# Kernel optimization log

Measured on AMD Instinct MI355X. Metric: run time of the kernel, lower is better.

Reference implementation:

```python
import jax, jax.numpy as jnp
import numpy as np

DIM_PROBLEM = 8192
DIM_CONTEXT = 512
DIM_HIDDEN = 1024


def setup_inputs() -> dict:
    key = jax.random.key(0)
    ks = jax.random.split(key, 8)
    s = 0.02
    H, C = DIM_HIDDEN, DIM_CONTEXT
    return {
        "context": jax.random.normal(ks[0], (C,), jnp.float32),
        # linear_1: dim_context -> 1
        "W1": jax.random.normal(ks[1], (1, C), jnp.float32) * s,
        "b1": jnp.zeros((1,), jnp.float32),
        # LSTM layer 0 (input dim 1), torch gate order [i, f, g, o]
        "Wih0": jax.random.normal(ks[2], (4 * H, 1), jnp.float32) * s,
        "Whh0": jax.random.normal(ks[3], (4 * H, H), jnp.float32) * s,
        "bih0": jnp.zeros((4 * H,), jnp.float32),
        "bhh0": jnp.zeros((4 * H,), jnp.float32),
        # LSTM layer 1 (input dim H)
        "Wih1": jax.random.normal(ks[4], (4 * H, H), jnp.float32) * s,
        "Whh1": jax.random.normal(ks[5], (4 * H, H), jnp.float32) * s,
        "bih1": jnp.zeros((4 * H,), jnp.float32),
        "bhh1": jnp.zeros((4 * H,), jnp.float32),
        # linear_2: dim_hidden -> 1
        "W2": jax.random.normal(ks[6], (1, H), jnp.float32) * s,
        "b2": jnp.zeros((1,), jnp.float32),
    }


def _lstm_cell(gin, h, c, Whh, b):
    # gin = W_ih @ x (precomputed); torch gate order i, f, g, o
    gates = gin + Whh @ h + b
    i, f, g, o = jnp.split(gates, 4)
    i, f, o = jax.nn.sigmoid(i), jax.nn.sigmoid(f), jax.nn.sigmoid(o)
    g = jnp.tanh(g)
    c = f * c + i * g
    return o * jnp.tanh(c), c


def reference(context, W1, b1, Wih0, Whh0, bih0, bhh0, Wih1, Whh1, bih1, bhh1, W2, b2):
    H = Whh0.shape[1]
    x0 = (W1 @ context + b1)[0]  # linear_1 seeds the first LSTM input (scalar)
    b0 = bih0 + bhh0
    b1g = bih1 + bhh1
    keys = jax.random.split(jax.random.key(42), DIM_PROBLEM)

    def step(carry, k):
        h0, c0, h1, c1, x, logp = carry
        h0, c0 = _lstm_cell(Wih0[:, 0] * x, h0, c0, Whh0, b0)
        h1, c1 = _lstm_cell(Wih1 @ h0, h1, c1, Whh1, b1g)
        p = jax.nn.sigmoid(W2 @ h1 + b2)[0]
        # Bernoulli sample; detached as in the original (.clone().detach(), .item())
        s = jax.lax.stop_gradient(jax.random.bernoulli(k, p).astype(jnp.float32))
        # log of running product  p^s * (1-p)^(1-s)
        logp = logp + s * jnp.log(p) + (1.0 - s) * jnp.log1p(-p)
        return (h0, c0, h1, c1, s, logp), s

    z = jnp.zeros((H,), jnp.float32)
    carry0 = (z, z, z, z, x0, jnp.float32(0.0))
    (_, _, _, _, _, logp), solution = jax.lax.scan(step, carry0, keys)
    return solution, logp
```

## Files before the change

kernel.cpp:

```cpp
#include <hip/hip_runtime.h>
#include <stdint.h>
#include <math.h>


#define H     1024
#define NSTEP 8192
#define NWG   512
#define BLK   64
#define NROW  25

typedef _Float16 h2 __attribute__((ext_vector_type(2)));
typedef _Float16 h8 __attribute__((ext_vector_type(8)));

union U32H2 { uint32_t u; h2 v; };

__device__ __forceinline__ unsigned long long pack_vt(float v0, float v1, uint32_t tag){
  U32H2 p; p.v.x = (_Float16)v0; p.v.y = (_Float16)v1;
  return ((unsigned long long)tag << 32) | (unsigned long long)p.u;
}

__device__ __forceinline__ uint2 tf2x32(uint32_t k0, uint32_t k1, uint32_t x0, uint32_t x1){
  uint32_t k2 = k0 ^ k1 ^ 0x1BD11BDAu;
  x0 += k0; x1 += k1;
#define TFR(r) { x0 += x1; x1 = (x1 << (r)) | (x1 >> (32 - (r))); x1 ^= x0; }
  TFR(13) TFR(15) TFR(26) TFR(6)
  x0 += k1; x1 += k2 + 1u;
  TFR(17) TFR(29) TFR(16) TFR(24)
  x0 += k2; x1 += k0 + 2u;
  TFR(13) TFR(15) TFR(26) TFR(6)
  x0 += k0; x1 += k1 + 3u;
  TFR(17) TFR(29) TFR(16) TFR(24)
  x0 += k1; x1 += k2 + 4u;
  TFR(13) TFR(15) TFR(26) TFR(6)
  x0 += k2; x1 += k0 + 5u;
#undef TFR
  uint2 r; r.x = x0; r.y = x1; return r;
}

__device__ __forceinline__ uint32_t jax_word(uint32_t i){
  return (i < 8192u) ? tf2x32(0u, 42u, i, i + 8192u).x
                     : tf2x32(0u, 42u, i - 8192u, i).y;
}

__device__ __forceinline__ float wred64(float x){
  #pragma unroll
  for(int off = 32; off > 0; off >>= 1) x += __shfl_xor(x, off, 64);
  return x;
}

#if __has_builtin(__builtin_amdgcn_fdot2)
__device__ __forceinline__ float fdot2f(h2 a, h2 b, float c){ return __builtin_amdgcn_fdot2(a, b, c, false); }
#else
__device__ __forceinline__ float fdot2f(h2 a, h2 b, float c){
  return (float)a.x * (float)b.x + (float)a.y * (float)b.y + c;
}
#endif

__device__ __forceinline__ float sigm(float x){
  x = fminf(fmaxf(x, -30.f), 30.f);
  return 1.f / (1.f + __expf(-x));
}
__device__ __forceinline__ float tanh_f(float x){
  x = fminf(fmaxf(x, -15.f), 15.f);
  float e = __expf(2.f * x);
  return (e - 1.f) / (e + 1.f);
}

__device__ __forceinline__ unsigned long long ld_slot(const unsigned long long* p){
  return __hip_atomic_load((unsigned long long*)p, __ATOMIC_RELAXED, __HIP_MEMORY_SCOPE_AGENT);
}

__device__ __forceinline__ void poll_h(const unsigned long long* __restrict__ buf,
                                       uint32_t tag, int lane, h2* hv){
  const unsigned long long* p0 = buf + (lane << 2);
  const unsigned long long* p1 = buf + 256 + (lane << 2);
  unsigned long long pv[8];
  #pragma unroll
  for(int k = 0; k < 4; k++) pv[k]     = ld_slot(p0 + k);
  #pragma unroll
  for(int k = 0; k < 4; k++) pv[4 + k] = ld_slot(p1 + k);
  #pragma unroll
  for(int k = 0; k < 8; k++){
    const unsigned long long* p = (k < 4) ? (p0 + k) : (p1 + (k - 4));
    while((uint32_t)(pv[k] >> 32) != tag){
      __builtin_amdgcn_s_sleep(1);
      pv[k] = ld_slot(p);
    }
  }
  #pragma unroll
  for(int k = 0; k < 8; k++){
    U32H2 u; u.u = (uint32_t)pv[k];
    hv[k] = u.v;
  }
}

__device__ __forceinline__ float row_part(const h2* __restrict__ wrow, int lane, const h2* hv){
  h8 wl = *(const h8*)(wrow + (lane << 2));
  h8 wh = *(const h8*)(wrow + 256 + (lane << 2));
  float a0 = 0.f, a1 = 0.f;
  h2 w;
  w = __builtin_shufflevector(wl, wl, 0, 1); a0 = fdot2f(w, hv[0], a0);
  w = __builtin_shufflevector(wl, wl, 2, 3); a1 = fdot2f(w, hv[1], a1);
  w = __builtin_shufflevector(wl, wl, 4, 5); a0 = fdot2f(w, hv[2], a0);
  w = __builtin_shufflevector(wl, wl, 6, 7); a1 = fdot2f(w, hv[3], a1);
  w = __builtin_shufflevector(wh, wh, 0, 1); a0 = fdot2f(w, hv[4], a0);
  w = __builtin_shufflevector(wh, wh, 2, 3); a1 = fdot2f(w, hv[5], a1);
  w = __builtin_shufflevector(wh, wh, 4, 5); a0 = fdot2f(w, hv[6], a0);
  w = __builtin_shufflevector(wh, wh, 6, 7); a1 = fdot2f(w, hv[7], a1);
  return a0 + a1;
}

__global__ void __launch_bounds__(BLK)
lstm_persist(const float* __restrict__ ctx,  const float* __restrict__ W1p,  const float* __restrict__ b1p,
             const float* __restrict__ Wih0, const float* __restrict__ Whh0,
             const float* __restrict__ bih0, const float* __restrict__ bhh0,
             const float* __restrict__ Wih1, const float* __restrict__ Whh1,
             const float* __restrict__ bih1, const float* __restrict__ bhh1,
             const float* __restrict__ W2p,  const float* __restrict__ b2p,
             float* __restrict__ out,
             unsigned long long* __restrict__ h0buf,
             unsigned long long* __restrict__ h1buf)
{
  __shared__ h2 w[NROW][H/2];

  const int lane = threadIdx.x;
  const int wg   = blockIdx.x;
  const int j0   = wg << 1;

  #pragma unroll 1
  for(int r = 0; r < NROW; r++){
    const float* rowp;
    if(r < 8)      { int g = r & 3,        j = j0 + (r >> 2);        rowp = Wih1 + (size_t)(g*H + j)*H; }
    else if(r < 16){ int rr = r - 8;  int g = rr & 3, j = j0 + (rr >> 2); rowp = Whh0 + (size_t)(g*H + j)*H; }
    else if(r < 24){ int rr = r - 16; int g = rr & 3, j = j0 + (rr >> 2); rowp = Whh1 + (size_t)(g*H + j)*H; }
    else           rowp = W2p;
    const float4* s4 = (const float4*)rowp;
    #pragma unroll
    for(int it = 0; it < 4; it++){
      float4 f = s4[lane + (it << 6)];
      h2 pa; pa.x = (_Float16)f.x; pa.y = (_Float16)f.y;
      h2 pb; pb.x = (_Float16)f.z; pb.y = (_Float16)f.w;
      const int ci = (lane + (it << 6)) << 1;
      w[r][ci] = pa; w[r][ci + 1] = pb;
    }
  }
  __syncthreads();

  float b0g[8], b1g[8], w0g[8];
  #pragma unroll
  for(int e = 0; e < 2; e++){
    const int j = j0 + e;
    #pragma unroll
    for(int g = 0; g < 4; g++){
      b0g[4*e + g] = bih0[g*H + j] + bhh0[g*H + j];
      b1g[4*e + g] = bih1[g*H + j] + bhh1[g*H + j];
      w0g[4*e + g] = Wih0[g*H + j];
    }
  }
  const float b2v = b2p[0];

  float xacc = 0.f;
  for(int c = lane; c < 512; c += 64) xacc += W1p[c] * ctx[c];
  const float x0 = wred64(xacc) + b1p[0];

  float c0[2], c1[2] = {0.f, 0.f}, logp = 0.f;
  float a0[8];
  float a1[8] = {0.f,0.f,0.f,0.f,0.f,0.f,0.f,0.f};

  {
    float h0v[2];
    #pragma unroll
    for(int e = 0; e < 2; e++){
      float gi = sigm (w0g[4*e+0]*x0 + b0g[4*e+0]);
      float gf = sigm (w0g[4*e+1]*x0 + b0g[4*e+1]);
      float gg = tanh_f(w0g[4*e+2]*x0 + b0g[4*e+2]);
      float go = sigm (w0g[4*e+3]*x0 + b0g[4*e+3]);
      c0[e] = gi * gg;
      h0v[e] = go * tanh_f(c0[e]);
    }
    if(lane == 0)
      __hip_atomic_store(&h0buf[wg], pack_vt(h0v[0], h0v[1], 1u),
                         __ATOMIC_RELAXED, __HIP_MEMORY_SCOPE_AGENT);
  }

  h2 hv[8];
  float u = 0.f;

  #pragma unroll 1
  for(int t = 0; t < NSTEP; t++){
    const uint32_t tt = (uint32_t)t;

    poll_h(h0buf, tt + 1u, lane, hv);

    float s1[8];
    #pragma unroll
    for(int r = 0; r < 8; r++) s1[r] = row_part(&w[r][0], lane, hv);
    #pragma unroll
    for(int off = 32; off > 0; off >>= 1){
      #pragma unroll
      for(int r = 0; r < 8; r++) s1[r] += __shfl_xor(s1[r], off, 64);
    }
    {
      float h1v[2];
      #pragma unroll
      for(int e = 0; e < 2; e++){
        float gi = sigm (s1[4*e+0] + a1[4*e+0] + b1g[4*e+0]);
        float gf = sigm (s1[4*e+1] + a1[4*e+1] + b1g[4*e+1]);
        float gg = tanh_f(s1[4*e+2] + a1[4*e+2] + b1g[4*e+2]);
        float go = sigm (s1[4*e+3] + a1[4*e+3] + b1g[4*e+3]);
        c1[e] = gf*c1[e] + gi*gg;
        h1v[e] = go * tanh_f(c1[e]);
      }
      if(lane == 0)
        __hip_atomic_store(&h1buf[wg], pack_vt(h1v[0], h1v[1], tt + 1u),
                           __ATOMIC_RELAXED, __HIP_MEMORY_SCOPE_AGENT);
    }

    {
      const uint32_t kk0 = jax_word(2u*tt), kk1 = jax_word(2u*tt + 1u);
      const uint32_t bits = tf2x32(kk0, kk1, 0u, 0u).x;
      u = __uint_as_float((bits >> 9) | 0x3f800000u) - 1.0f;
    }
    float sa[8];
    #pragma unroll
    for(int r = 0; r < 8; r++) sa[r] = row_part(&w[8 + r][0], lane, hv);
    #pragma unroll
    for(int off = 32; off > 0; off >>= 1){
      #pragma unroll
      for(int r = 0; r < 8; r++) sa[r] += __shfl_xor(sa[r], off, 64);
    }
    #pragma unroll
    for(int r = 0; r < 8; r++) a0[r] = sa[r];

    poll_h(h1buf, tt + 1u, lane, hv);

    float z = row_part(&w[24][0], lane, hv);
    z = wred64(z) + b2v;
    const float p = sigm(z);
    const float s = (u < p) ? 1.f : 0.f;
    logp += s * __logf(p) + (1.f - s) * __logf(1.f - p);
    if(wg == 0 && lane == 0) out[t] = s;
    {
      float h0v[2];
      #pragma unroll
      for(int e = 0; e < 2; e++){
        float gi = sigm (a0[4*e+0] + w0g[4*e+0]*s + b0g[4*e+0]);
        float gf = sigm (a0[4*e+1] + w0g[4*e+1]*s + b0g[4*e+1]);
        float gg = tanh_f(a0[4*e+2] + w0g[4*e+2]*s + b0g[4*e+2]);
        float go = sigm (a0[4*e+3] + w0g[4*e+3]*s + b0g[4*e+3]);
        c0[e] = gf*c0[e] + gi*gg;
        h0v[e] = go * tanh_f(c0[e]);
      }
      if(lane == 0)
        __hip_atomic_store(&h0buf[wg], pack_vt(h0v[0], h0v[1], tt + 2u),
                           __ATOMIC_RELAXED, __HIP_MEMORY_SCOPE_AGENT);
    }

    float sb[8];
    #pragma unroll
    for(int r = 0; r < 8; r++) sb[r] = row_part(&w[16 + r][0], lane, hv);
    #pragma unroll
    for(int off = 32; off > 0; off >>= 1){
      #pragma unroll
      for(int r = 0; r < 8; r++) sb[r] += __shfl_xor(sb[r], off, 64);
    }
    #pragma unroll
    for(int r = 0; r < 8; r++) a1[r] = sb[r];
  }

  if(wg == 0 && lane == 0) out[NSTEP] = logp;
}

extern "C" void kernel_launch(void* const* d_in, const int* in_sizes, int n_in,
                              void* d_out, int out_size, void* d_ws, size_t ws_size,
                              hipStream_t stream){
  unsigned long long* h0buf = (unsigned long long*)d_ws;
  unsigned long long* h1buf = h0buf + 512;
  hipLaunchKernelGGL(lstm_persist, dim3(NWG), dim3(BLK), 0, stream,
    (const float*)d_in[0],  (const float*)d_in[1],  (const float*)d_in[2],
    (const float*)d_in[3],  (const float*)d_in[4],  (const float*)d_in[5],  (const float*)d_in[6],
    (const float*)d_in[7],  (const float*)d_in[8],  (const float*)d_in[9],  (const float*)d_in[10],
    (const float*)d_in[11], (const float*)d_in[12],
    (float*)d_out, h0buf, h1buf);
}
```

Baseline: 33.45 ms.

## Speculate layer-0 state for both sample outcomes to remove one grid sync per step

Each step, every workgroup now computes the next layer-0 hidden state for both possible Bernoulli outcomes (s=0 and s=1) and publishes both copies, tagged, to double-buffered slots. After the sample is drawn, each workgroup picks the matching copy. This takes the layer-0 exchange off the serial chain from h1 to the sample, so each step needs one cross-workgroup wait on the critical path instead of two. The Wih1·h0 and Whh1·h1 matvecs are also merged into a single reduction. In exchange, layer-0 gate math is done twice and more global slots are polled per step.

```diff
diff --git a/kernel.cpp b/kernel.cpp
--- a/kernel.cpp
+++ b/kernel.cpp
@@ -70,6 +70,28 @@
   return __hip_atomic_load((unsigned long long*)p, __ATOMIC_RELAXED, __HIP_MEMORY_SCOPE_AGENT);
 }
 
+__device__ __forceinline__ void spin8(unsigned long long* pv,
+                                      const unsigned long long* p0,
+                                      const unsigned long long* p1,
+                                      uint32_t tag){
+  #pragma unroll
+  for(int k = 0; k < 8; k++){
+    const unsigned long long* p = (k < 4) ? (p0 + k) : (p1 + (k - 4));
+    while((uint32_t)(pv[k] >> 32) != tag){
+      __builtin_amdgcn_s_sleep(1);
+      pv[k] = ld_slot(p);
+    }
+  }
+}
+
+__device__ __forceinline__ void unpack8(const unsigned long long* pv, h2* hv){
+  #pragma unroll
+  for(int k = 0; k < 8; k++){
+    U32H2 u; u.u = (uint32_t)pv[k];
+    hv[k] = u.v;
+  }
+}
+
 __device__ __forceinline__ void poll_h(const unsigned long long* __restrict__ buf,
                                        uint32_t tag, int lane, h2* hv){
   const unsigned long long* p0 = buf + (lane << 2);
@@ -79,19 +101,8 @@
   for(int k = 0; k < 4; k++) pv[k]     = ld_slot(p0 + k);
   #pragma unroll
   for(int k = 0; k < 4; k++) pv[4 + k] = ld_slot(p1 + k);
-  #pragma unroll
-  for(int k = 0; k < 8; k++){
-    const unsigned long long* p = (k < 4) ? (p0 + k) : (p1 + (k - 4));
-    while((uint32_t)(pv[k] >> 32) != tag){
-      __builtin_amdgcn_s_sleep(1);
-      pv[k] = ld_slot(p);
-    }
-  }
-  #pragma unroll
-  for(int k = 0; k < 8; k++){
-    U32H2 u; u.u = (uint32_t)pv[k];
-    hv[k] = u.v;
-  }
+  spin8(pv, p0, p1, tag);
+  unpack8(pv, hv);
 }
 
 __device__ __forceinline__ float row_part(const h2* __restrict__ wrow, int lane, const h2* hv){
@@ -118,8 +129,9 @@
              const float* __restrict__ bih1, const float* __restrict__ bhh1,
              const float* __restrict__ W2p,  const float* __restrict__ b2p,
              float* __restrict__ out,
-             unsigned long long* __restrict__ h0buf,
-             unsigned long long* __restrict__ h1buf)
+             unsigned long long* __restrict__ h0boot,
+             unsigned long long* __restrict__ h1base,
+             unsigned long long* __restrict__ cbase)
 {
   __shared__ h2 w[NROW][H/2];
 
@@ -164,8 +176,7 @@
   const float x0 = wred64(xacc) + b1p[0];
 
   float c0[2], c1[2] = {0.f, 0.f}, logp = 0.f;
-  float a0[8];
-  float a1[8] = {0.f,0.f,0.f,0.f,0.f,0.f,0.f,0.f};
+  float c0A[2], c0B[2];
 
   {
     float h0v[2];
@@ -175,97 +186,184 @@
       float gf = sigm (w0g[4*e+1]*x0 + b0g[4*e+1]);
       float gg = tanh_f(w0g[4*e+2]*x0 + b0g[4*e+2]);
       float go = sigm (w0g[4*e+3]*x0 + b0g[4*e+3]);
+      (void)gf;
       c0[e] = gi * gg;
       h0v[e] = go * tanh_f(c0[e]);
     }
     if(lane == 0)
-      __hip_atomic_store(&h0buf[wg], pack_vt(h0v[0], h0v[1], 1u),
+      __hip_atomic_store(&h0boot[wg], pack_vt(h0v[0], h0v[1], 1u),
                          __ATOMIC_RELAXED, __HIP_MEMORY_SCOPE_AGENT);
   }
 
   h2 hv[8];
-  float u = 0.f;
+  poll_h(h0boot, 1u, lane, hv);
+
+  {
+    float s1[8];
+    #pragma unroll
+    for(int r = 0; r < 8; r++) s1[r] = row_part(&w[r][0], lane, hv);
+    #pragma unroll
+    for(int off = 32; off > 0; off >>= 1){
+      #pragma unroll
+      for(int r = 0; r < 8; r++) s1[r] += __shfl_xor(s1[r], off, 64);
+    }
+    float h1vv[2];
+    #pragma unroll
+    for(int e = 0; e < 2; e++){
+      float gi = sigm (s1[4*e+0] + b1g[4*e+0]);
+      float gf = sigm (s1[4*e+1] + b1g[4*e+1]);
+      float gg = tanh_f(s1[4*e+2] + b1g[4*e+2]);
+      float go = sigm (s1[4*e+3] + b1g[4*e+3]);
+      c1[e] = gf*c1[e] + gi*gg;
+      h1vv[e] = go * tanh_f(c1[e]);
+    }
+    if(lane == 0)
+      __hip_atomic_store(h1base + 512 + wg, pack_vt(h1vv[0], h1vv[1], 1u),
+                         __ATOMIC_RELAXED, __HIP_MEMORY_SCOPE_AGENT);
+  }
+
+  {
+    float a0v[8];
+    #pragma unroll
+    for(int r = 0; r < 8; r++) a0v[r] = row_part(&w[8 + r][0], lane, hv);
+    #pragma unroll
+    for(int off = 32; off > 0; off >>= 1){
+      #pragma unroll
+      for(int r = 0; r < 8; r++) a0v[r] += __shfl_xor(a0v[r], off, 64);
+    }
+    float hA[2], hB[2];
+    #pragma unroll
+    for(int e = 0; e < 2; e++){
+      float gi = sigm (a0v[4*e+0] + b0g[4*e+0]);
+      float gf = sigm (a0v[4*e+1] + b0g[4*e+1]);
+      float gg = tanh_f(a0v[4*e+2] + b0g[4*e+2]);
+      float go = sigm (a0v[4*e+3] + b0g[4*e+3]);
+      c0A[e] = gf*c0[e] + gi*gg; hA[e] = go * tanh_f(c0A[e]);
+      float gi1 = sigm (a0v[4*e+0] + w0g[4*e+0] + b0g[4*e+0]);
+      float gf1 = sigm (a0v[4*e+1] + w0g[4*e+1] + b0g[4*e+1]);
+      float gg1 = tanh_f(a0v[4*e+2] + w0g[4*e+2] + b0g[4*e+2]);
+      float go1 = sigm (a0v[4*e+3] + w0g[4*e+3] + b0g[4*e+3]);
+      c0B[e] = gf1*c0[e] + gi1*gg1; hB[e] = go1 * tanh_f(c0B[e]);
+    }
+    if(lane == 0){
+      __hip_atomic_store(cbase + wg,       pack_vt(hA[0], hA[1], 2u),
+                         __ATOMIC_RELAXED, __HIP_MEMORY_SCOPE_AGENT);
+      __hip_atomic_store(cbase + 512 + wg, pack_vt(hB[0], hB[1], 2u),
+                         __ATOMIC_RELAXED, __HIP_MEMORY_SCOPE_AGENT);
+    }
+  }
 
   #pragma unroll 1
   for(int t = 0; t < NSTEP; t++){
-    const uint32_t tt = (uint32_t)t;
-
-    poll_h(h0buf, tt + 1u, lane, hv);
-
-    float s1[8];
-    #pragma unroll
-    for(int r = 0; r < 8; r++) s1[r] = row_part(&w[r][0], lane, hv);
+    const uint32_t tagH = (uint32_t)t + 1u;
+    const uint32_t tagC = (uint32_t)t + 2u;
+    const unsigned long long* h1b = h1base + ((size_t)(tagH & 1u) << 9);
+    const unsigned long long* cAb = cbase  + ((size_t)(tagC & 1u) << 10);
+    const unsigned long long* cBb = cAb + 512;
+
+    const unsigned long long* hp0 = h1b + (lane << 2);
+    const unsigned long long* hp1 = h1b + 256 + (lane << 2);
+    const unsigned long long* ap0 = cAb + (lane << 2);
+    const unsigned long long* ap1 = cAb + 256 + (lane << 2);
+    const unsigned long long* bp0 = cBb + (lane << 2);
+    const unsigned long long* bp1 = cBb + 256 + (lane << 2);
+
+    unsigned long long pH[8], pA[8], pB[8];
+    #pragma unroll
+    for(int k = 0; k < 4; k++){
+      pH[k] = ld_slot(hp0 + k); pH[4 + k] = ld_slot(hp1 + k);
+      pA[k] = ld_slot(ap0 + k); pA[4 + k] = ld_slot(ap1 + k);
+      pB[k] = ld_slot(bp0 + k); pB[4 + k] = ld_slot(bp1 + k);
+    }
+
+    float u;
+    {
+      const uint32_t kk0 = jax_word(2u*(uint32_t)t), kk1 = jax_word(2u*(uint32_t)t + 1u);
+      const uint32_t bits = tf2x32(kk0, kk1, 0u, 0u).x;
+      u = __uint_as_float((bits >> 9) | 0x3f800000u) - 1.0f;
+    }
+
+    spin8(pH, hp0, hp1, tagH);
+    h2 hv1[8]; unpack8(pH, hv1);
+
+    float z = row_part(&w[24][0], lane, hv1);
+    z = wred64(z) + b2v;
+    const float p = sigm(z);
+    const float sv = (u < p) ? 1.f : 0.f;
+    logp += sv * __logf(p) + (1.f - sv) * __logf(1.f - p);
+    if(wg == 0 && lane == 0) out[t] = sv;
+
+    const bool sb = (sv != 0.f);
+    {
+      const unsigned long long* sp0 = sb ? bp0 : ap0;
+      const unsigned long long* sp1 = sb ? bp1 : ap1;
+      unsigned long long ps[8];
+      #pragma unroll
+      for(int k = 0; k < 8; k++) ps[k] = sb ? pB[k] : pA[k];
+      spin8(ps, sp0, sp1, tagC);
+      unpack8(ps, hv);
+    }
+    #pragma unroll
+    for(int e = 0; e < 2; e++) c0[e] = sb ? c0B[e] : c0A[e];
+
+    float rr[16];
+    #pragma unroll
+    for(int r = 0; r < 8; r++) rr[r]     = row_part(&w[r][0],      lane, hv);
+    #pragma unroll
+    for(int r = 0; r < 8; r++) rr[8 + r] = row_part(&w[16 + r][0], lane, hv1);
     #pragma unroll
     for(int off = 32; off > 0; off >>= 1){
       #pragma unroll
-      for(int r = 0; r < 8; r++) s1[r] += __shfl_xor(s1[r], off, 64);
+      for(int r = 0; r < 16; r++) rr[r] += __shfl_xor(rr[r], off, 64);
     }
     {
-      float h1v[2];
+      float h1vv[2];
       #pragma unroll
       for(int e = 0; e < 2; e++){
-        float gi = sigm (s1[4*e+0] + a1[4*e+0] + b1g[4*e+0]);
-        float gf = sigm (s1[4*e+1] + a1[4*e+1] + b1g[4*e+1]);
-        float gg = tanh_f(s1[4*e+2] + a1[4*e+2] + b1g[4*e+2]);
-        float go = sigm (s1[4*e+3] + a1[4*e+3] + b1g[4*e+3]);
+        float gi = sigm (rr[4*e+0] + rr[8+4*e+0] + b1g[4*e+0]);
+        float gf = sigm (rr[4*e+1] + rr[8+4*e+1] + b1g[4*e+1]);
+        float gg = tanh_f(rr[4*e+2] + rr[8+4*e+2] + b1g[4*e+2]);
+        float go = sigm (rr[4*e+3] + rr[8+4*e+3] + b1g[4*e+3]);
         c1[e] = gf*c1[e] + gi*gg;
-        h1v[e] = go * tanh_f(c1[e]);
+        h1vv[e] = go * tanh_f(c1[e]);
       }
       if(lane == 0)
-        __hip_atomic_store(&h1buf[wg], pack_vt(h1v[0], h1v[1], tt + 1u),
+        __hip_atomic_store(h1base + ((size_t)(tagC & 1u) << 9) + wg,
+                           pack_vt(h1vv[0], h1vv[1], tagC),
                            __ATOMIC_RELAXED, __HIP_MEMORY_SCOPE_AGENT);
     }
 
     {
-      const uint32_t kk0 = jax_word(2u*tt), kk1 = jax_word(2u*tt + 1u);
-      const uint32_t bits = tf2x32(kk0, kk1, 0u, 0u).x;
-      u = __uint_as_float((bits >> 9) | 0x3f800000u) - 1.0f;
-    }
-    float sa[8];
-    #pragma unroll
-    for(int r = 0; r < 8; r++) sa[r] = row_part(&w[8 + r][0], lane, hv);
-    #pragma unroll
-    for(int off = 32; off > 0; off >>= 1){
-      #pragma unroll
-      for(int r = 0; r < 8; r++) sa[r] += __shfl_xor(sa[r], off, 64);
-    }
-    #pragma unroll
-    for(int r = 0; r < 8; r++) a0[r] = sa[r];
-
-    poll_h(h1buf, tt + 1u, lane, hv);
-
-    float z = row_part(&w[24][0], lane, hv);
-    z = wred64(z) + b2v;
-    const float p = sigm(z);
-    const float s = (u < p) ? 1.f : 0.f;
-    logp += s * __logf(p) + (1.f - s) * __logf(1.f - p);
-    if(wg == 0 && lane == 0) out[t] = s;
-    {
-      float h0v[2];
+      float a0v[8];
+      #pragma unroll
+      for(int r = 0; r < 8; r++) a0v[r] = row_part(&w[8 + r][0], lane, hv);
+      #pragma unroll
+      for(int off = 32; off > 0; off >>= 1){
+        #pragma unroll
+        for(int r = 0; r < 8; r++) a0v[r] += __shfl_xor(a0v[r], off, 64);
+      }
+      float hA[2], hB[2];
       #pragma unroll
       for(int e = 0; e < 2; e++){
-        float gi = sigm (a0[4*e+0] + w0g[4*e+0]*s + b0g[4*e+0]);
-        float gf = sigm (a0[4*e+1] + w0g[4*e+1]*s + b0g[4*e+1]);
-        float gg = tanh_f(a0[4*e+2] + w0g[4*e+2]*s + b0g[4*e+2]);
-        float go = sigm (a0[4*e+3] + w0g[4*e+3]*s + b0g[4*e+3]);
-        c0[e] = gf*c0[e] + gi*gg;
-        h0v[e] = go * tanh_f(c0[e]);
+        float gi = sigm (a0v[4*e+0] + b0g[4*e+0]);
+        float gf = sigm (a0v[4*e+1] + b0g[4*e+1]);
+        float gg = tanh_f(a0v[4*e+2] + b0g[4*e+2]);
+        float go = sigm (a0v[4*e+3] + b0g[4*e+3]);
+        c0A[e] = gf*c0[e] + gi*gg; hA[e] = go * tanh_f(c0A[e]);
+        float gi1 = sigm (a0v[4*e+0] + w0g[4*e+0] + b0g[4*e+0]);
+        float gf1 = sigm (a0v[4*e+1] + w0g[4*e+1] + b0g[4*e+1]);
+        float gg1 = tanh_f(a0v[4*e+2] + w0g[4*e+2] + b0g[4*e+2]);
+        float go1 = sigm (a0v[4*e+3] + w0g[4*e+3] + b0g[4*e+3]);
+        c0B[e] = gf1*c0[e] + gi1*gg1; hB[e] = go1 * tanh_f(c0B[e]);
       }
-      if(lane == 0)
-        __hip_atomic_store(&h0buf[wg], pack_vt(h0v[0], h0v[1], tt + 2u),
+      if(lane == 0){
+        unsigned long long* cp = cbase + ((size_t)(tagH & 1u) << 10);
+        __hip_atomic_store(cp + wg,       pack_vt(hA[0], hA[1], tagC + 1u),
                            __ATOMIC_RELAXED, __HIP_MEMORY_SCOPE_AGENT);
-    }
-
-    float sb[8];
-    #pragma unroll
-    for(int r = 0; r < 8; r++) sb[r] = row_part(&w[16 + r][0], lane, hv);
-    #pragma unroll
-    for(int off = 32; off > 0; off >>= 1){
-      #pragma unroll
-      for(int r = 0; r < 8; r++) sb[r] += __shfl_xor(sb[r], off, 64);
-    }
-    #pragma unroll
-    for(int r = 0; r < 8; r++) a1[r] = sb[r];
+        __hip_atomic_store(cp + 512 + wg, pack_vt(hB[0], hB[1], tagC + 1u),
+                           __ATOMIC_RELAXED, __HIP_MEMORY_SCOPE_AGENT);
+      }
+    }
   }
 
   if(wg == 0 && lane == 0) out[NSTEP] = logp;
@@ -274,12 +372,14 @@
 extern "C" void kernel_launch(void* const* d_in, const int* in_sizes, int n_in,
                               void* d_out, int out_size, void* d_ws, size_t ws_size,
                               hipStream_t stream){
-  unsigned long long* h0buf = (unsigned long long*)d_ws;
-  unsigned long long* h1buf = h0buf + 512;
+  unsigned long long* ws = (unsigned long long*)d_ws;
+  unsigned long long* h0boot = ws;
+  unsigned long long* h1base = ws + 512;
+  unsigned long long* cbase  = ws + 1536;
   hipLaunchKernelGGL(lstm_persist, dim3(NWG), dim3(BLK), 0, stream,
     (const float*)d_in[0],  (const float*)d_in[1],  (const float*)d_in[2],
     (const float*)d_in[3],  (const float*)d_in[4],  (const float*)d_in[5],  (const float*)d_in[6],
     (const float*)d_in[7],  (const float*)d_in[8],  (const float*)d_in[9],  (const float*)d_in[10],
     (const float*)d_in[11], (const float*)d_in[12],
-    (float*)d_out, h0buf, h1buf);
-}
+    (float*)d_out, h0boot, h1base, cbase);
+}
```

Measured after the change: 76.61 ms. +129.0%, slower.
